# Optimization experiments

Measured on AMD Instinct MI355X. Metric: run time of the kernel, lower is better.

The kernel has to match this reference:

```python
import jax, jax.numpy as jnp
import numpy as np

S_LIST = (0.015, 0.02, 0.04, 0.08)
EPS = 1e-6
LOG_EPS = float(np.log(EPS))


def _ema_filtfilt(x, s):
    """scipy.signal.filtfilt([s], [1, s-1], x, axis=-1, padtype=None).

    Forward pass: y[n] = (1-s)*y[n-1] + s*x[n], with scipy's lfilter_zi*x[0]
    initial condition, which makes y[0] = x[0] exactly. Then the same filter
    is run backward (flip, filter, flip), again with y2[0] = (flipped y)[0].
    Implemented as a parallel linear-recurrence via associative_scan.
    """
    def one_pass(v):
        a = jnp.full_like(v, 1.0 - s).at[..., 0].set(0.0)
        b = (s * v).at[..., 0].set(v[..., 0])
        def comb(c1, c2):
            a1, b1 = c1
            a2, b2 = c2
            return a1 * a2, b1 * a2 + b2
        _, y = jax.lax.associative_scan(comb, (a, b), axis=-1)
        return y

    y = one_pass(x)                       # forward
    y = jnp.flip(one_pass(jnp.flip(y, axis=-1)), axis=-1)  # backward
    return y


def setup_inputs() -> dict:
    key = jax.random.key(0)
    ks = jax.random.split(key, 5)
    B, C, F, T = 16, 1, 256, 4096
    K = len(S_LIST)
    x = jax.random.uniform(ks[0], (B, C, F, T), dtype=jnp.float32)
    log_alpha = jnp.log(jax.random.normal(ks[1], (F,), dtype=jnp.float32) * 0.1 + 1.0)
    log_delta = jnp.log(jax.random.normal(ks[2], (F,), dtype=jnp.float32) * 0.1 + 1.0)
    log_r = jnp.log(jax.random.normal(ks[3], (F,), dtype=jnp.float32) * 0.1 + 1.0)
    z_ks = jax.random.normal(ks[4], (K, F), dtype=jnp.float32) * 0.1 + np.log(1.0 / K)
    return {"x": x, "log_alpha": log_alpha, "log_delta": log_delta,
            "log_r": log_r, "z_ks": z_ks}


def reference(x, log_alpha, log_delta, log_r, z_ks):
    # per-frequency params broadcast over [B, C, F, T]
    alpha = jnp.exp(log_alpha)[None, None, :, None]
    delta = jnp.exp(log_delta)[None, None, :, None]
    r = jnp.exp(log_r)[None, None, :, None]
    ez = jnp.exp(z_ks)
    w_ks = ez / jnp.sum(ez)  # [K, F], normalized over ALL entries (as in source)

    # multi-scale filtfilt smoothers; scipy path is detached from autodiff
    smoothers = jnp.stack([_ema_filtfilt(x, s) for s in S_LIST])  # [K,B,C,F,T]
    smoothers = jax.lax.stop_gradient(smoothers)

    M = jnp.einsum('kf,kbcft->bcft', w_ks, smoothers)
    M = jnp.exp(-alpha * (LOG_EPS + jnp.log1p(M / EPS)))
    return (x * M + delta) ** r - delta ** r
```

## Files before the change

kernel.cpp:

```cpp
#include <hip/hip_runtime.h>
#include <math.h>

#define T_DIM 4096
#define F_DIM 256
#define NROWS 4096
#define CHUNK 16
#define LOG2E 1.4426950408889634f

typedef float v2f __attribute__((ext_vector_type(2)));

__device__ __forceinline__ float fexp2(float v) { return __builtin_amdgcn_exp2f(v); }
__device__ __forceinline__ float flog2(float v) { return __builtin_amdgcn_logf(v); }
__device__ __forceinline__ float fexp(float v)  { return fexp2(v * LOG2E); }

__host__ __device__ constexpr float cpow(float b, int e) {
    float r = 1.0f;
    for (int i = 0; i < e; ++i) r *= b;
    return r;
}

template<int N> struct PT { float v[N]; };
template<int N>
__host__ __device__ constexpr PT<N> mk_pows(float a) {
    PT<N> t{}; float p = 1.0f;
    for (int i = 0; i < N; ++i) { t.v[i] = p; p *= a; }
    return t;
}

__device__ __forceinline__ v2f shfl_up2(v2f v, int d) {
    v2f r; r.x = __shfl_up(v.x, d, 64); r.y = __shfl_up(v.y, d, 64); return r;
}
__device__ __forceinline__ v2f shfl_down2(v2f v, int d) {
    v2f r; r.x = __shfl_down(v.x, d, 64); r.y = __shfl_down(v.y, d, 64); return r;
}

#define S0 0.015f
#define S1 0.02f
#define S2 0.04f
#define S3 0.08f

__global__ __launch_bounds__(256, 4)
void pcen_kernel(const float* __restrict__ x,
                 const float* __restrict__ log_alpha,
                 const float* __restrict__ log_delta,
                 const float* __restrict__ log_r,
                 const float* __restrict__ z_ks,
                 float* __restrict__ out)
{
#pragma clang fp contract(fast)
    const int tid  = threadIdx.x;
    const int lane = tid & 63;
    const int wid  = tid >> 6;
    const int rid  = blockIdx.x;
    const int f    = rid & (F_DIM - 1);

    __shared__ v2f sE0f[4], sE1f[4];
    __shared__ v2f sE0b[4], sE1b[4];

    const size_t base = (size_t)rid * T_DIM + (size_t)tid * CHUNK;
    const float4* xp = (const float4*)(x + base);
    float4 xq0 = xp[0], xq1 = xp[1], xq2 = xp[2], xq3 = xp[3];

    const float v_la = log_alpha[f];
    const float v_ld = log_delta[f];
    const float v_lr = log_r[f];
    float zf[4];
    #pragma unroll
    for (int k = 0; k < 4; ++k) zf[k] = z_ks[k * F_DIM + f];

    float zs = 0.0f;
    #pragma unroll
    for (int j = 0; j < 16; ++j) zs += fexp(z_ks[lane + 64 * j]);
    #pragma unroll
    for (int d = 1; d < 64; d <<= 1) zs += __shfl_xor(zs, d, 64);
    const float invsum = 1.0f / zs;

    float wk[4];
    #pragma unroll
    for (int k = 0; k < 4; ++k) wk[k] = fexp(zf[k]) * invsum;
    const float alpha = fexp(v_la);
    const float delta = fexp(v_ld);
    const float rr    = fexp(v_lr);
    const float dr    = fexp2(rr * flog2(delta));
    const float nalpha = -alpha;

    float xv[CHUNK];
    xv[0]=xq0.x; xv[1]=xq0.y; xv[2]=xq0.z; xv[3]=xq0.w;
    xv[4]=xq1.x; xv[5]=xq1.y; xv[6]=xq1.z; xv[7]=xq1.w;
    xv[8]=xq2.x; xv[9]=xq2.y; xv[10]=xq2.z; xv[11]=xq2.w;
    xv[12]=xq3.x; xv[13]=xq3.y; xv[14]=xq3.z; xv[15]=xq3.w;

    constexpr float a0 = 1.0f - S0, a1 = 1.0f - S1, a2 = 1.0f - S2, a3 = 1.0f - S3;
    constexpr float A0 = cpow(a0, CHUNK), A1 = cpow(a1, CHUNK);
    constexpr float A2 = cpow(a2, CHUNK), A3 = cpow(a3, CHUNK);
    constexpr float A64_0 = cpow(a0, 64*CHUNK), A64_1 = cpow(a1, 64*CHUNK);
    constexpr float A64_2 = cpow(a2, 64*CHUNK), A64_3 = cpow(a3, 64*CHUNK);
    constexpr PT<CHUNK+1> P0 = mk_pows<CHUNK+1>(a0);
    constexpr PT<CHUNK+1> P1 = mk_pows<CHUNK+1>(a1);
    constexpr PT<CHUNK+1> P2 = mk_pows<CHUNK+1>(a2);
    constexpr PT<CHUNK+1> P3 = mk_pows<CHUNK+1>(a3);
    constexpr PT<33> PA0 = mk_pows<33>(A0);
    constexpr PT<33> PA1 = mk_pows<33>(A1);
    constexpr PT<33> PA2 = mk_pows<33>(A2);
    constexpr PT<33> PA3 = mk_pows<33>(A3);

    const v2f av01 = {a0, a1}, av23 = {a2, a3};
    const v2f sv01 = {S0, S1}, sv23 = {S2, S3};
    const v2f A64v01 = {A64_0, A64_1}, A64v23 = {A64_2, A64_3};
    const float lgA0 = flog2(A0), lgA1 = flog2(A1), lgA2 = flog2(A2), lgA3 = flog2(A3);
    const v2f zero = {0.0f, 0.0f};

    v2f y0[CHUNK], y1[CHUNK];

    {
        v2f x0v = {xv[0], xv[0]};
        y0[0] = (tid == 0) ? x0v : (sv01 * x0v);
        y1[0] = (tid == 0) ? x0v : (sv23 * x0v);
    }
    #pragma unroll
    for (int i = 1; i < CHUNK; ++i) {
        v2f xi = {xv[i], xv[i]};
        y0[i] = av01 * y0[i-1] + sv01 * xi;
        y1[i] = av23 * y1[i-1] + sv23 * xi;
    }
    {
        v2f e0 = y0[CHUNK-1], e1 = y1[CHUNK-1];
        #pragma unroll
        for (int st = 0; st < 6; ++st) {
            const int d = 1 << st;
            const v2f Ad01 = {PA0.v[d], PA1.v[d]};
            const v2f Ad23 = {PA2.v[d], PA3.v[d]};
            v2f t0 = shfl_up2(e0, d);
            v2f t1 = shfl_up2(e1, d);
            if (lane >= d) { e0 = Ad01 * t0 + e0; e1 = Ad23 * t1 + e1; }
        }
        if (lane == 63) { sE0f[wid] = e0; sE1f[wid] = e1; }
        __syncthreads();
        v2f C0 = zero, C1 = zero;
        for (int j = 0; j < wid; ++j) {
            C0 = A64v01 * C0 + sE0f[j];
            C1 = A64v23 * C1 + sE1f[j];
        }
        v2f ex0 = shfl_up2(e0, 1), ex1 = shfl_up2(e1, 1);
        v2f cp0 = (lane == 0) ? zero : ex0;
        v2f cp1 = (lane == 0) ? zero : ex1;
        const float fl = (float)lane;
        v2f pAl01 = {fexp2(fl * lgA0), fexp2(fl * lgA1)};
        v2f pAl23 = {fexp2(fl * lgA2), fexp2(fl * lgA3)};
        v2f c0 = cp0 + pAl01 * C0;
        v2f c1 = cp1 + pAl23 * C1;
        #pragma unroll
        for (int i = 0; i < CHUNK; ++i) {
            const v2f ap01 = {P0.v[i+1], P1.v[i+1]};
            const v2f ap23 = {P2.v[i+1], P3.v[i+1]};
            y0[i] = ap01 * c0 + y0[i];
            y1[i] = ap23 * c1 + y1[i];
        }
    }

    y0[CHUNK-1] = (tid == 255) ? y0[CHUNK-1] : (sv01 * y0[CHUNK-1]);
    y1[CHUNK-1] = (tid == 255) ? y1[CHUNK-1] : (sv23 * y1[CHUNK-1]);
    #pragma unroll
    for (int i = CHUNK-2; i >= 0; --i) {
        y0[i] = av01 * y0[i+1] + sv01 * y0[i];
        y1[i] = av23 * y1[i+1] + sv23 * y1[i];
    }
    {
        v2f e0 = y0[0], e1 = y1[0];
        #pragma unroll
        for (int st = 0; st < 6; ++st) {
            const int d = 1 << st;
            const v2f Ad01 = {PA0.v[d], PA1.v[d]};
            const v2f Ad23 = {PA2.v[d], PA3.v[d]};
            v2f t0 = shfl_down2(e0, d);
            v2f t1 = shfl_down2(e1, d);
            if (lane < 64 - d) { e0 = Ad01 * t0 + e0; e1 = Ad23 * t1 + e1; }
        }
        if (lane == 0) { sE0b[wid] = e0; sE1b[wid] = e1; }
        __syncthreads();
        v2f C0 = zero, C1 = zero;
        for (int j = 3; j > wid; --j) {
            C0 = A64v01 * C0 + sE0b[j];
            C1 = A64v23 * C1 + sE1b[j];
        }
        v2f ex0 = shfl_down2(e0, 1), ex1 = shfl_down2(e1, 1);
        v2f cn0 = (lane == 63) ? zero : ex0;
        v2f cn1 = (lane == 63) ? zero : ex1;
        const float frl = (float)(63 - lane);
        v2f pAr01 = {fexp2(frl * lgA0), fexp2(frl * lgA1)};
        v2f pAr23 = {fexp2(frl * lgA2), fexp2(frl * lgA3)};
        v2f c0 = cn0 + pAr01 * C0;
        v2f c1 = cn1 + pAr23 * C1;
        #pragma unroll
        for (int i = CHUNK-1; i >= 0; --i) {
            const v2f ap01 = {P0.v[CHUNK-i], P1.v[CHUNK-i]};
            const v2f ap23 = {P2.v[CHUNK-i], P3.v[CHUNK-i]};
            y0[i] = ap01 * c0 + y0[i];
            y1[i] = ap23 * c1 + y1[i];
        }
    }

    float4* op = (float4*)(out + base);
    const v2f wv01 = {wk[0], wk[1]}, wv23 = {wk[2], wk[3]};
    #pragma unroll
    for (int j = 0; j < 4; ++j) {
        float o[4];
        #pragma unroll
        for (int q = 0; q < 4; ++q) {
            const int i = 4*j + q;
            v2f mp = wv01 * y0[i] + wv23 * y1[i];
            const float M  = mp.x + mp.y;
            const float Mp = fexp2(nalpha * flog2(M + 1.0e-6f));
            const float v  = fmaf(xv[i], Mp, delta);
            o[q] = fexp2(rr * flog2(v)) - dr;
        }
        op[j] = make_float4(o[0], o[1], o[2], o[3]);
    }
}

extern "C" void kernel_launch(void* const* d_in, const int* in_sizes, int n_in,
                              void* d_out, int out_size, void* d_ws, size_t ws_size,
                              hipStream_t stream) {
    const float* x  = (const float*)d_in[0];
    const float* la = (const float*)d_in[1];
    const float* ld = (const float*)d_in[2];
    const float* lr = (const float*)d_in[3];
    const float* zk = (const float*)d_in[4];
    float* o = (float*)d_out;
    (void)in_sizes; (void)n_in; (void)out_size; (void)d_ws; (void)ws_size;
    hipLaunchKernelGGL(pcen_kernel, dim3(NROWS), dim3(256), 0, stream,
                       x, la, ld, lr, zk, o);
}
```

Baseline: 39.48 us.

## Decompose filtfilt into independent forward and anti-causal passes with single barrier

Rewrites the forward-then-backward EMA as a causal pass on x plus an anti-causal pass on x with closed-form coefficients (s/(1-a^2), s^2/(1-a^2)) and boundary terms. This lets the forward and backward chunk scans and wave scans run together, sharing one __syncthreads instead of two. It also stores only a 16-float weighted accumulator instead of 64 per-scale values, and spreads the z_ks softmax normalisation across the block. The risk is that the algebraic decomposition must reproduce scipy's boundary conditions exactly, and the summed terms may lose some precision.

```diff
diff --git a/kernel.cpp b/kernel.cpp
--- a/kernel.cpp
+++ b/kernel.cpp
@@ -54,13 +54,15 @@
     const int rid  = blockIdx.x;
     const int f    = rid & (F_DIM - 1);
 
-    __shared__ v2f sE0f[4], sE1f[4];
-    __shared__ v2f sE0b[4], sE1b[4];
-
-    const size_t base = (size_t)rid * T_DIM + (size_t)tid * CHUNK;
+    __shared__ float sred[4];
+    __shared__ v2f sEf0[4], sEf1[4];
+    __shared__ v2f sEb0[4], sEb1[4];
+
+    const size_t rbase = (size_t)rid * T_DIM;
+    const size_t base  = rbase + (size_t)tid * CHUNK;
     const float4* xp = (const float4*)(x + base);
     float4 xq0 = xp[0], xq1 = xp[1], xq2 = xp[2], xq3 = xp[3];
-
+    const float x0bc = x[rbase];
     const float v_la = log_alpha[f];
     const float v_ld = log_delta[f];
     const float v_lr = log_r[f];
@@ -68,149 +70,154 @@
     #pragma unroll
     for (int k = 0; k < 4; ++k) zf[k] = z_ks[k * F_DIM + f];
 
-    float zs = 0.0f;
-    #pragma unroll
-    for (int j = 0; j < 16; ++j) zs += fexp(z_ks[lane + 64 * j]);
-    #pragma unroll
-    for (int d = 1; d < 64; d <<= 1) zs += __shfl_xor(zs, d, 64);
-    const float invsum = 1.0f / zs;
-
-    float wk[4];
-    #pragma unroll
-    for (int k = 0; k < 4; ++k) wk[k] = fexp(zf[k]) * invsum;
+    float zs = fexp(z_ks[tid])       + fexp(z_ks[tid + 256])
+             + fexp(z_ks[tid + 512]) + fexp(z_ks[tid + 768]);
+    #pragma unroll
+    for (int d = 32; d >= 1; d >>= 1) zs += __shfl_down(zs, d, 64);
+    if (lane == 0) sred[wid] = zs;
+
+    float xv[CHUNK];
+    xv[0]=xq0.x; xv[1]=xq0.y; xv[2]=xq0.z; xv[3]=xq0.w;
+    xv[4]=xq1.x; xv[5]=xq1.y; xv[6]=xq1.z; xv[7]=xq1.w;
+    xv[8]=xq2.x; xv[9]=xq2.y; xv[10]=xq2.z; xv[11]=xq2.w;
+    xv[12]=xq3.x; xv[13]=xq3.y; xv[14]=xq3.z; xv[15]=xq3.w;
+
+    float ez[4];
+    #pragma unroll
+    for (int k = 0; k < 4; ++k) ez[k] = fexp(zf[k]);
     const float alpha = fexp(v_la);
     const float delta = fexp(v_ld);
     const float rr    = fexp(v_lr);
     const float dr    = fexp2(rr * flog2(delta));
     const float nalpha = -alpha;
 
-    float xv[CHUNK];
-    xv[0]=xq0.x; xv[1]=xq0.y; xv[2]=xq0.z; xv[3]=xq0.w;
-    xv[4]=xq1.x; xv[5]=xq1.y; xv[6]=xq1.z; xv[7]=xq1.w;
-    xv[8]=xq2.x; xv[9]=xq2.y; xv[10]=xq2.z; xv[11]=xq2.w;
-    xv[12]=xq3.x; xv[13]=xq3.y; xv[14]=xq3.z; xv[15]=xq3.w;
-
     constexpr float a0 = 1.0f - S0, a1 = 1.0f - S1, a2 = 1.0f - S2, a3 = 1.0f - S3;
     constexpr float A0 = cpow(a0, CHUNK), A1 = cpow(a1, CHUNK);
     constexpr float A2 = cpow(a2, CHUNK), A3 = cpow(a3, CHUNK);
-    constexpr float A64_0 = cpow(a0, 64*CHUNK), A64_1 = cpow(a1, 64*CHUNK);
-    constexpr float A64_2 = cpow(a2, 64*CHUNK), A64_3 = cpow(a3, 64*CHUNK);
-    constexpr PT<CHUNK+1> P0 = mk_pows<CHUNK+1>(a0);
-    constexpr PT<CHUNK+1> P1 = mk_pows<CHUNK+1>(a1);
-    constexpr PT<CHUNK+1> P2 = mk_pows<CHUNK+1>(a2);
-    constexpr PT<CHUNK+1> P3 = mk_pows<CHUNK+1>(a3);
+    constexpr float AW0 = cpow(a0, 64*CHUNK), AW1 = cpow(a1, 64*CHUNK);
+    constexpr float AW2 = cpow(a2, 64*CHUNK), AW3 = cpow(a3, 64*CHUNK);
     constexpr PT<33> PA0 = mk_pows<33>(A0);
     constexpr PT<33> PA1 = mk_pows<33>(A1);
     constexpr PT<33> PA2 = mk_pows<33>(A2);
     constexpr PT<33> PA3 = mk_pows<33>(A3);
+    constexpr float C1_0 = S0/(1.0f-a0*a0), C1_1 = S1/(1.0f-a1*a1);
+    constexpr float C1_2 = S2/(1.0f-a2*a2), C1_3 = S3/(1.0f-a3*a3);
+    constexpr float C2_0 = S0*S0/(1.0f-a0*a0), C2_1 = S1*S1/(1.0f-a1*a1);
+    constexpr float C2_2 = S2*S2/(1.0f-a2*a2), C2_3 = S3*S3/(1.0f-a3*a3);
 
     const v2f av01 = {a0, a1}, av23 = {a2, a3};
     const v2f sv01 = {S0, S1}, sv23 = {S2, S3};
-    const v2f A64v01 = {A64_0, A64_1}, A64v23 = {A64_2, A64_3};
+    const v2f AWv01 = {AW0, AW1}, AWv23 = {AW2, AW3};
     const float lgA0 = flog2(A0), lgA1 = flog2(A1), lgA2 = flog2(A2), lgA3 = flog2(A3);
     const v2f zero = {0.0f, 0.0f};
 
-    v2f y0[CHUNK], y1[CHUNK];
-
+    v2f ef0, ef1, eb0, eb1;
     {
-        v2f x0v = {xv[0], xv[0]};
-        y0[0] = (tid == 0) ? x0v : (sv01 * x0v);
-        y1[0] = (tid == 0) ? x0v : (sv23 * x0v);
-    }
-    #pragma unroll
-    for (int i = 1; i < CHUNK; ++i) {
-        v2f xi = {xv[i], xv[i]};
-        y0[i] = av01 * y0[i-1] + sv01 * xi;
-        y1[i] = av23 * y1[i-1] + sv23 * xi;
-    }
+        v2f xa = {xv[0],  xv[0]};
+        v2f xb = {xv[15], xv[15]};
+        ef0 = sv01 * xa;  ef1 = sv23 * xa;
+        eb0 = sv01 * xb;  eb1 = sv23 * xb;
+        #pragma unroll
+        for (int i = 1; i < CHUNK; ++i) {
+            v2f xi = {xv[i],    xv[i]};
+            v2f xj = {xv[15-i], xv[15-i]};
+            ef0 = av01 * ef0 + sv01 * xi;
+            ef1 = av23 * ef1 + sv23 * xi;
+            eb0 = av01 * eb0 + sv01 * xj;
+            eb1 = av23 * eb1 + sv23 * xj;
+        }
+    }
+
+    #pragma unroll
+    for (int st = 0; st < 6; ++st) {
+        const int d = 1 << st;
+        const v2f Ad01 = {PA0.v[d], PA1.v[d]};
+        const v2f Ad23 = {PA2.v[d], PA3.v[d]};
+        v2f tf0 = shfl_up2(ef0, d);
+        v2f tf1 = shfl_up2(ef1, d);
+        v2f tb0 = shfl_down2(eb0, d);
+        v2f tb1 = shfl_down2(eb1, d);
+        if (lane >= d)      { ef0 = Ad01 * tf0 + ef0; ef1 = Ad23 * tf1 + ef1; }
+        if (lane < 64 - d)  { eb0 = Ad01 * tb0 + eb0; eb1 = Ad23 * tb1 + eb1; }
+    }
+    v2f exf0 = shfl_up2(ef0, 1),  exf1 = shfl_up2(ef1, 1);
+    v2f exb0 = shfl_down2(eb0, 1), exb1 = shfl_down2(eb1, 1);
+
+    if (lane == 63) { sEf0[wid] = ef0; sEf1[wid] = ef1; }
+    if (lane == 0)  { sEb0[wid] = eb0; sEb1[wid] = eb1; }
+    __syncthreads();
+
+    const float invsum = 1.0f / (sred[0] + sred[1] + sred[2] + sred[3]);
+    const float wk0 = ez[0]*invsum, wk1 = ez[1]*invsum, wk2 = ez[2]*invsum, wk3 = ez[3]*invsum;
+    const v2f wf01 = {wk0*C1_0, wk1*C1_1};
+    const v2f wf23 = {wk2*C1_2, wk3*C1_3};
+    const float W2 = wk0*C2_0 + wk1*C2_1 + wk2*C2_2 + wk3*C2_3;
+
+    const v2f x0v = {x0bc, x0bc};
+    v2f Cf0 = x0v, Cf1 = x0v;
+    for (int j = 0; j < wid; ++j) {
+        Cf0 = AWv01 * Cf0 + sEf0[j];
+        Cf1 = AWv23 * Cf1 + sEf1[j];
+    }
+    v2f yT0 = x0v, yT1 = x0v;
+    #pragma unroll
+    for (int j = 0; j < 4; ++j) {
+        yT0 = AWv01 * yT0 + sEf0[j];
+        yT1 = AWv23 * yT1 + sEf1[j];
+    }
+    v2f Cb0 = yT0, Cb1 = yT1;
+    for (int j = 3; j > wid; --j) {
+        Cb0 = AWv01 * Cb0 + sEb0[j];
+        Cb1 = AWv23 * Cb1 + sEb1[j];
+    }
+
+    const float fl  = (float)lane;
+    const float frl = (float)(63 - lane);
+    v2f pAl01 = {fexp2(fl * lgA0),  fexp2(fl * lgA1)};
+    v2f pAl23 = {fexp2(fl * lgA2),  fexp2(fl * lgA3)};
+    v2f pAr01 = {fexp2(frl * lgA0), fexp2(frl * lgA1)};
+    v2f pAr23 = {fexp2(frl * lgA2), fexp2(frl * lgA3)};
+    v2f cpf0 = (lane == 0) ? zero : exf0;
+    v2f cpf1 = (lane == 0) ? zero : exf1;
+    v2f cnb0 = (lane == 63) ? zero : exb0;
+    v2f cnb1 = (lane == 63) ? zero : exb1;
+    v2f cf0 = cpf0 + pAl01 * Cf0;
+    v2f cf1 = cpf1 + pAl23 * Cf1;
+    v2f cb0 = cnb0 + pAr01 * Cb0;
+    v2f cb1 = cnb1 + pAr23 * Cb1;
+
+    float Macc[CHUNK];
     {
-        v2f e0 = y0[CHUNK-1], e1 = y1[CHUNK-1];
-        #pragma unroll
-        for (int st = 0; st < 6; ++st) {
-            const int d = 1 << st;
-            const v2f Ad01 = {PA0.v[d], PA1.v[d]};
-            const v2f Ad23 = {PA2.v[d], PA3.v[d]};
-            v2f t0 = shfl_up2(e0, d);
-            v2f t1 = shfl_up2(e1, d);
-            if (lane >= d) { e0 = Ad01 * t0 + e0; e1 = Ad23 * t1 + e1; }
-        }
-        if (lane == 63) { sE0f[wid] = e0; sE1f[wid] = e1; }
-        __syncthreads();
-        v2f C0 = zero, C1 = zero;
-        for (int j = 0; j < wid; ++j) {
-            C0 = A64v01 * C0 + sE0f[j];
-            C1 = A64v23 * C1 + sE1f[j];
-        }
-        v2f ex0 = shfl_up2(e0, 1), ex1 = shfl_up2(e1, 1);
-        v2f cp0 = (lane == 0) ? zero : ex0;
-        v2f cp1 = (lane == 0) ? zero : ex1;
-        const float fl = (float)lane;
-        v2f pAl01 = {fexp2(fl * lgA0), fexp2(fl * lgA1)};
-        v2f pAl23 = {fexp2(fl * lgA2), fexp2(fl * lgA3)};
-        v2f c0 = cp0 + pAl01 * C0;
-        v2f c1 = cp1 + pAl23 * C1;
+        v2f yf0 = cf0, yf1 = cf1;
         #pragma unroll
         for (int i = 0; i < CHUNK; ++i) {
-            const v2f ap01 = {P0.v[i+1], P1.v[i+1]};
-            const v2f ap23 = {P2.v[i+1], P3.v[i+1]};
-            y0[i] = ap01 * c0 + y0[i];
-            y1[i] = ap23 * c1 + y1[i];
-        }
-    }
-
-    y0[CHUNK-1] = (tid == 255) ? y0[CHUNK-1] : (sv01 * y0[CHUNK-1]);
-    y1[CHUNK-1] = (tid == 255) ? y1[CHUNK-1] : (sv23 * y1[CHUNK-1]);
-    #pragma unroll
-    for (int i = CHUNK-2; i >= 0; --i) {
-        y0[i] = av01 * y0[i+1] + sv01 * y0[i];
-        y1[i] = av23 * y1[i+1] + sv23 * y1[i];
+            v2f xi = {xv[i], xv[i]};
+            yf0 = av01 * yf0 + sv01 * xi;
+            yf1 = av23 * yf1 + sv23 * xi;
+            v2f mp = wf01 * yf0 + wf23 * yf1;
+            Macc[i] = mp.x + mp.y;
+        }
     }
     {
-        v2f e0 = y0[0], e1 = y1[0];
-        #pragma unroll
-        for (int st = 0; st < 6; ++st) {
-            const int d = 1 << st;
-            const v2f Ad01 = {PA0.v[d], PA1.v[d]};
-            const v2f Ad23 = {PA2.v[d], PA3.v[d]};
-            v2f t0 = shfl_down2(e0, d);
-            v2f t1 = shfl_down2(e1, d);
-            if (lane < 64 - d) { e0 = Ad01 * t0 + e0; e1 = Ad23 * t1 + e1; }
-        }
-        if (lane == 0) { sE0b[wid] = e0; sE1b[wid] = e1; }
-        __syncthreads();
-        v2f C0 = zero, C1 = zero;
-        for (int j = 3; j > wid; --j) {
-            C0 = A64v01 * C0 + sE0b[j];
-            C1 = A64v23 * C1 + sE1b[j];
-        }
-        v2f ex0 = shfl_down2(e0, 1), ex1 = shfl_down2(e1, 1);
-        v2f cn0 = (lane == 63) ? zero : ex0;
-        v2f cn1 = (lane == 63) ? zero : ex1;
-        const float frl = (float)(63 - lane);
-        v2f pAr01 = {fexp2(frl * lgA0), fexp2(frl * lgA1)};
-        v2f pAr23 = {fexp2(frl * lgA2), fexp2(frl * lgA3)};
-        v2f c0 = cn0 + pAr01 * C0;
-        v2f c1 = cn1 + pAr23 * C1;
+        v2f zb0 = cb0, zb1 = cb1;
         #pragma unroll
         for (int i = CHUNK-1; i >= 0; --i) {
-            const v2f ap01 = {P0.v[CHUNK-i], P1.v[CHUNK-i]};
-            const v2f ap23 = {P2.v[CHUNK-i], P3.v[CHUNK-i]};
-            y0[i] = ap01 * c0 + y0[i];
-            y1[i] = ap23 * c1 + y1[i];
+            v2f xi = {xv[i], xv[i]};
+            zb0 = av01 * zb0 + sv01 * xi;
+            zb1 = av23 * zb1 + sv23 * xi;
+            v2f mp = wf01 * zb0 + wf23 * zb1;
+            Macc[i] = Macc[i] + (mp.x + mp.y) - W2 * xv[i];
         }
     }
 
     float4* op = (float4*)(out + base);
-    const v2f wv01 = {wk[0], wk[1]}, wv23 = {wk[2], wk[3]};
     #pragma unroll
     for (int j = 0; j < 4; ++j) {
         float o[4];
         #pragma unroll
         for (int q = 0; q < 4; ++q) {
             const int i = 4*j + q;
-            v2f mp = wv01 * y0[i] + wv23 * y1[i];
-            const float M  = mp.x + mp.y;
-            const float Mp = fexp2(nalpha * flog2(M + 1.0e-6f));
+            const float Mp = fexp2(nalpha * flog2(Macc[i] + 1.0e-6f));
             const float v  = fmaf(xv[i], Mp, delta);
             o[q] = fexp2(rr * flog2(v)) - dr;
         }
```

After: 37.42 us. -5.2%, faster.
